# Kernel tuning notes

Measured on AMD Instinct MI355X. Metric: run time of the kernel, lower is better.

## Reference

```python
import jax, jax.numpy as jnp
import numpy as np

B, N, HID = 1, 2048, 1024
H, WK, WV = 16, 64, 64
DH = HID // H  # 64


def setup_inputs() -> dict:
    key = jax.random.key(0)
    ks = jax.random.split(key, 10)
    s = 0.02
    return {
        "hidden_states": jax.random.normal(ks[0], (B, N, HID), jnp.float32),
        "attention_mask": jnp.ones((B, N), jnp.float32),
        "Wq": jax.random.normal(ks[1], (HID, HID), jnp.float32) * s,
        "bq": jnp.zeros((HID,), jnp.float32),
        "Wk": jax.random.normal(ks[2], (HID, HID), jnp.float32) * s,
        "bk": jnp.zeros((HID,), jnp.float32),
        "Wv": jax.random.normal(ks[3], (HID, HID), jnp.float32) * s,
        "bv": jnp.zeros((HID,), jnp.float32),
        # Conv1D(2*WK+1, DH, bias=False): weight [nx=DH, nf=2*WK+1]
        "W_rel_k": jax.random.normal(ks[4], (DH, 2 * WK + 1), jnp.float32) * s,
        # relative_pos_val: [2*WV+1, DH]
        "W_rel_v": jax.random.normal(ks[5], (2 * WV + 1, DH), jnp.float32) * s,
    }


def _attention(hidden_states, attention_mask, Wq, bq, Wk, bk, Wv, bv, W_rel_k, W_rel_v):
    b, n, _ = hidden_states.shape

    def heads(x):  # [B,N,HID] -> [B,H,N,DH]
        return x.reshape(b, n, H, DH).transpose(0, 2, 1, 3)

    q = heads(hidden_states @ Wq + bq)
    k = heads(hidden_states @ Wk + bk)
    v = heads(hidden_states @ Wv + bv)

    scores = jnp.einsum("bhid,bhjd->bhij", q, k)  # [B,H,N,N]

    # --- relative-position key bias: bias[i, j] = q_i . w_{j-i+WK} for |j-i|<=WK ---
    a_k = jnp.einsum("bhid,dw->bhiw", q, W_rel_k)  # [B,H,N,2*WK+1]
    rows = jnp.arange(n)
    slot = rows[None, :] - rows[:, None] + WK       # [N,N] relative slot j-i+WK
    valid_k = (slot >= 0) & (slot <= 2 * WK)
    bias = a_k[:, :, rows[:, None], jnp.clip(slot, 0, 2 * WK)]  # [B,H,N,N]
    scores = scores + jnp.where(valid_k, bias, 0.0)

    scores = scores / np.float32(np.sqrt(DH))  # temperature == 1.0

    # extended attention mask: (1 - mask) * dtype_min added to scores
    ext = (1.0 - attention_mask)[:, None, None, :] * jnp.finfo(scores.dtype).min
    scores = scores + ext

    probs = jax.nn.softmax(scores, axis=-1)  # [B,H,N,N]

    ctx = jnp.einsum("bhij,bhjd->bhid", probs, v)  # [B,H,N,DH]

    # --- relative-position value: band[i, r] = probs[i, i-WV+r]; ctx += band @ W_rel_v ---
    offs = jnp.arange(2 * WV + 1)
    kpos = rows[:, None] - WV + offs[None, :]       # [N, 2*WV+1] absolute key position
    valid_v = (kpos >= 0) & (kpos < n)
    band = probs[:, :, rows[:, None], jnp.clip(kpos, 0, n - 1)]  # [B,H,N,2*WV+1]
    band = jnp.where(valid_v, band, 0.0)
    ctx = ctx + jnp.einsum("bhiw,wd->bhid", band, W_rel_v)

    # merge heads -> [B,N,HID]
    return ctx.transpose(0, 2, 1, 3).reshape(b, n, HID)


def reference(hidden_states, attention_mask, Wq, bq, Wk, bk, Wv, bv, W_rel_k, W_rel_v):
    return _attention(hidden_states, attention_mask, Wq, bq, Wk, bk, Wv, bv, W_rel_k, W_rel_v)
```

## Files before the change

kernel.cpp:

```cpp
#include <hip/hip_runtime.h>
#include <hip/hip_bf16.h>

#define NSEQ 2048
#define HIDDIM 1024
#define NH 16
#define DHEAD 64
#define NW 129
#define AKS 132

typedef float          f32x4 __attribute__((ext_vector_type(4)));
typedef _Float16       f16x4 __attribute__((ext_vector_type(4)));
typedef _Float16       f16x8 __attribute__((ext_vector_type(8)));
typedef unsigned short u16x8 __attribute__((ext_vector_type(8)));
typedef unsigned short u16;

__device__ __forceinline__ float b2f(u16 u){ return __uint_as_float(((unsigned)u) << 16); }
__device__ __forceinline__ float ld_any(const void* p, long idx, int flag){
  return flag ? b2f(((const u16*)p)[idx]) : ((const float*)p)[idx];
}

static const size_t OFF_Q    = 0;
static const size_t OFF_K    = (size_t)4  << 20;
static const size_t OFF_VT   = (size_t)8  << 20;
static const size_t OFF_WT   = (size_t)12 << 20;
static const size_t OFF_AK   = (size_t)18 << 20;
static const size_t OFF_M    = OFF_AK + (size_t)NH * NSEQ * AKS * 4;
static const size_t OFF_L    = OFF_M + (size_t)2 * NH * NSEQ * 4;
static const size_t OFF_CTXP = OFF_L + (size_t)2 * NH * NSEQ * 4;
static const size_t OFF_HSF  = OFF_CTXP + (size_t)2 * NSEQ * HIDDIM * 4;
static const size_t OFF_BIAS = OFF_HSF + (size_t)NSEQ * HIDDIM * 2;
static const size_t OFF_WRK  = OFF_BIAS + 3 * 1024 * 4;
static const size_t OFF_WRV  = OFF_WRK + (size_t)DHEAD * NW * 4;
static const size_t OFF_EXT  = OFF_WRV + (size_t)NW * DHEAD * 4;
static const size_t OFF_FLAG = OFF_EXT + (size_t)NSEQ * 4;

__global__ void detect_kernel(const unsigned* __restrict__ mask_raw, int* __restrict__ flagp){
  *flagp = (mask_raw[0] == 0x3F800000u) ? 0 : 1;
}

__global__ void cvt_hs_kernel(const void* __restrict__ hs, const int* __restrict__ flagp,
                              _Float16* __restrict__ hsf){
  const int flag = *flagp;
  const long base = (long)(blockIdx.x * 256 + threadIdx.x) * 8;
  f16x8 o;
  if (flag){
    const u16* b = (const u16*)hs;
#pragma unroll
    for (int e = 0; e < 8; e++) o[e] = (_Float16)b2f(b[base + e]);
  } else {
    const float* f = (const float*)hs;
#pragma unroll
    for (int e = 0; e < 8; e++) o[e] = (_Float16)f[base + e];
  }
  *(f16x8*)(hsf + base) = o;
}

__global__ void cvt_small_kernel(const void* __restrict__ bq, const void* __restrict__ bk,
                                 const void* __restrict__ bv, const void* __restrict__ wrk,
                                 const void* __restrict__ wrv, const void* __restrict__ mask,
                                 const int* __restrict__ flagp,
                                 float* __restrict__ biasf, float* __restrict__ wrkf,
                                 float* __restrict__ wrvf, float* __restrict__ extf){
  const int flag = *flagp;
  const int idx = blockIdx.x * 256 + threadIdx.x;
  if (idx < 1024)            biasf[idx] = ld_any(bq, idx, flag);
  else if (idx < 2048)       biasf[idx] = ld_any(bk, idx - 1024, flag);
  else if (idx < 3072)       biasf[idx] = ld_any(bv, idx - 2048, flag);
  else if (idx < 3072 + 8256)  wrkf[idx - 3072]  = ld_any(wrk, idx - 3072, flag);
  else if (idx < 3072 + 16512) wrvf[idx - 11328] = ld_any(wrv, idx - 11328, flag);
  else if (idx < 3072 + 16512 + 2048)
    extf[idx - 19584] = (1.f - ld_any(mask, idx - 19584, flag)) * -1.0e30f;
}

__global__ void wtrans_kernel(const void* __restrict__ Wq, const void* __restrict__ Wk,
                              const void* __restrict__ Wv, const int* __restrict__ flagp,
                              _Float16* __restrict__ Wt){
  __shared__ __attribute__((aligned(16))) _Float16 tile[64][65];
  const int flag = *flagp;
  const int z = blockIdx.z;
  const void* src = (z == 0) ? Wq : ((z == 1) ? Wk : Wv);
  _Float16* dst = Wt + (size_t)z * 1024 * 1024;
  const int o0 = blockIdx.x * 64, k0 = blockIdx.y * 64;
  const int t = threadIdx.x;
#pragma unroll
  for (int c = 0; c < 2; c++){
    int idx = t + 256 * c;
    int r = idx >> 3, c8 = (idx & 7) * 8;
    long off = (long)(k0 + r) * 1024 + o0 + c8;
#pragma unroll
    for (int e = 0; e < 8; e++) tile[r][c8 + e] = (_Float16)ld_any(src, off + e, flag);
  }
  __syncthreads();
#pragma unroll
  for (int c = 0; c < 2; c++){
    int idx = t + 256 * c;
    int orow = idx >> 3, k8 = (idx & 7) * 8;
    f16x8 v;
#pragma unroll
    for (int e = 0; e < 8; e++) v[e] = tile[k8 + e][orow];
    *(f16x8*)(dst + (size_t)(o0 + orow) * 1024 + k0 + k8) = v;
  }
}

__launch_bounds__(256, 2)
__global__ void qkv_kernel(const _Float16* __restrict__ hsf, const _Float16* __restrict__ Wt,
                           const float* __restrict__ biasf,
                           _Float16* __restrict__ Qf, _Float16* __restrict__ Kf,
                           _Float16* __restrict__ Vtf){
  __shared__ __attribute__((aligned(16))) _Float16 As[128 * 40];
  __shared__ __attribute__((aligned(16))) _Float16 Bs[128 * 40];
  const int z = blockIdx.z;
  const _Float16* Wz = Wt + (size_t)z * 1024 * 1024;
  const int o0 = blockIdx.x * 128, m0 = blockIdx.y * 128;
  const int t = threadIdx.x, lane = t & 63, wave = t >> 6;
  const int wm = wave >> 1, wn = wave & 1;
  const int q = lane >> 4, ln = lane & 15;
  f32x4 acc[4][4];
#pragma unroll
  for (int a = 0; a < 4; a++)
#pragma unroll
    for (int b = 0; b < 4; b++) acc[a][b] = (f32x4){0.f, 0.f, 0.f, 0.f};

  for (int k0 = 0; k0 < 1024; k0 += 32){
#pragma unroll
    for (int c = 0; c < 2; c++){
      int idx = t + 256 * c;
      int r = idx >> 2, col = (idx & 3) * 8;
      *(f16x8*)&As[r * 40 + col] = *(const f16x8*)(hsf + (size_t)(m0 + r) * 1024 + k0 + col);
      *(f16x8*)&Bs[r * 40 + col] = *(const f16x8*)(Wz + (size_t)(o0 + r) * 1024 + k0 + col);
    }
    __syncthreads();
    f16x8 af[4], bf[4];
#pragma unroll
    for (int mt = 0; mt < 4; mt++) af[mt] = *(const f16x8*)&As[(wm * 64 + mt * 16 + ln) * 40 + q * 8];
#pragma unroll
    for (int nt = 0; nt < 4; nt++) bf[nt] = *(const f16x8*)&Bs[(wn * 64 + nt * 16 + ln) * 40 + q * 8];
#pragma unroll
    for (int mt = 0; mt < 4; mt++)
#pragma unroll
      for (int nt = 0; nt < 4; nt++)
        acc[mt][nt] = __builtin_amdgcn_mfma_f32_16x16x32_f16(af[mt], bf[nt], acc[mt][nt], 0, 0, 0);
    __syncthreads();
  }
#pragma unroll
  for (int nt = 0; nt < 4; nt++){
    int o = o0 + wn * 64 + nt * 16 + ln;
    float bval = biasf[z * 1024 + o];
    int hh = o >> 6, dd = o & 63;
#pragma unroll
    for (int mt = 0; mt < 4; mt++){
      int nb = m0 + wm * 64 + mt * 16 + q * 4;
      if (z == 2){
        f16x4 pk;
#pragma unroll
        for (int r = 0; r < 4; r++) pk[r] = (_Float16)(acc[mt][nt][r] + bval);
        *(f16x4*)(Vtf + (size_t)(hh * 64 + dd) * 2048 + nb) = pk;
      } else {
        _Float16* dstp = (z == 0) ? Qf : Kf;
#pragma unroll
        for (int r = 0; r < 4; r++)
          dstp[(size_t)(hh * 2048 + nb + r) * 64 + dd] = (_Float16)(acc[mt][nt][r] + bval);
      }
    }
  }
}

__launch_bounds__(256, 2)
__global__ void ak_kernel(const _Float16* __restrict__ Qf, const float* __restrict__ wrkf,
                          float* __restrict__ ak){
  __shared__ __attribute__((aligned(16))) _Float16 WrkT[144 * 72];
  const int h = blockIdx.y;
  const int i0 = blockIdx.x * 128;
  const int t = threadIdx.x, lane = t & 63, wave = t >> 6;
  const int q = lane >> 4, ln = lane & 15;
  for (int c = 0; c < 36; c++){
    int idx = t + 256 * c;
    int w = idx >> 6, d = idx & 63;
    float v = (w < NW) ? wrkf[d * NW + w] : 0.f;
    WrkT[w * 72 + d] = (_Float16)v;
  }
  __syncthreads();
  f16x8 afr[2][2];
#pragma unroll
  for (int mt = 0; mt < 2; mt++){
    int row = i0 + wave * 32 + mt * 16 + ln;
#pragma unroll
    for (int ks = 0; ks < 2; ks++)
      afr[mt][ks] = *(const f16x8*)(Qf + (size_t)(h * 2048 + row) * 64 + ks * 32 + q * 8);
  }
  f32x4 acc[2][9];
#pragma unroll
  for (int a = 0; a < 2; a++)
#pragma unroll
    for (int b = 0; b < 9; b++) acc[a][b] = (f32x4){0.f, 0.f, 0.f, 0.f};
#pragma unroll
  for (int nt = 0; nt < 9; nt++){
    f16x8 bfr0 = *(const f16x8*)&WrkT[(nt * 16 + ln) * 72 + q * 8];
    f16x8 bfr1 = *(const f16x8*)&WrkT[(nt * 16 + ln) * 72 + 32 + q * 8];
#pragma unroll
    for (int mt = 0; mt < 2; mt++){
      acc[mt][nt] = __builtin_amdgcn_mfma_f32_16x16x32_f16(afr[mt][0], bfr0, acc[mt][nt], 0, 0, 0);
      acc[mt][nt] = __builtin_amdgcn_mfma_f32_16x16x32_f16(afr[mt][1], bfr1, acc[mt][nt], 0, 0, 0);
    }
  }
#pragma unroll
  for (int nt = 0; nt < 9; nt++){
    int w = nt * 16 + ln;
    if (w > 128) continue;
#pragma unroll
    for (int mt = 0; mt < 2; mt++){
      int ib = i0 + wave * 32 + mt * 16 + q * 4;
#pragma unroll
      for (int r = 0; r < 4; r++)
        ak[(size_t)(h * 2048 + ib + r) * AKS + w] = acc[mt][nt][r];
    }
  }
}

__launch_bounds__(256, 4)
__global__ void flash_kernel(const float* __restrict__ extf,
                             const _Float16* __restrict__ Qf, const _Float16* __restrict__ Kf,
                             const _Float16* __restrict__ Vtf, float* akm,
                             float* __restrict__ ctxpart, float* __restrict__ mws,
                             float* __restrict__ lws){
  __shared__ __attribute__((aligned(16))) _Float16 Ks[128 * 72];
  __shared__ __attribute__((aligned(16))) _Float16 Vts[64 * 136];
  __shared__ __attribute__((aligned(16))) float exts[128];
  const int h = blockIdx.x, qt = blockIdx.y, jh = blockIdx.z;
  const int t = threadIdx.x, lane = t & 63, wave = t >> 6;
  const int q = lane >> 4, ln = lane & 15;
  const int ibase = qt * 64 + wave * 16;
  const int i = ibase + ln;
  f16x8 qfrag[2];
  {
    const _Float16* qrow = Qf + (size_t)(h * 2048 + i) * 64;
    qfrag[0] = *(const f16x8*)(qrow + q * 8);
    qfrag[1] = *(const f16x8*)(qrow + 32 + q * 8);
  }
  f32x4 accc[4];
#pragma unroll
  for (int dt = 0; dt < 4; dt++) accc[dt] = (f32x4){0.f, 0.f, 0.f, 0.f};
  float m_i = -1.0e30f, l_i = 0.f;
  float* akrow = akm + (size_t)(h * 2048 + i) * AKS;

  for (int jt = 0; jt < 8; jt++){
    const int j0 = jh * 1024 + jt * 128;
#pragma unroll
    for (int c = 0; c < 4; c++){
      int idx = t + 256 * c;
      {
        int row = idx >> 3, col = idx & 7;
        *(f16x8*)&Ks[row * 72 + col * 8] =
            *(const f16x8*)(Kf + (size_t)(h * 2048 + j0 + row) * 64 + col * 8);
      }
      {
        int row = idx >> 4, col = idx & 15;
        *(f16x8*)&Vts[row * 136 + col * 8] =
            *(const f16x8*)(Vtf + (size_t)(h * 64 + row) * 2048 + j0 + col * 8);
      }
    }
    if (t < 128) exts[t] = extf[j0 + t];
    __syncthreads();
    f32x4 s[8];
#pragma unroll
    for (int mt = 0; mt < 8; mt++){
      f16x8 kf0 = *(const f16x8*)&Ks[(mt * 16 + ln) * 72 + q * 8];
      f16x8 kf1 = *(const f16x8*)&Ks[(mt * 16 + ln) * 72 + 32 + q * 8];
      f32x4 zz = (f32x4){0.f, 0.f, 0.f, 0.f};
      zz = __builtin_amdgcn_mfma_f32_16x16x32_f16(kf0, qfrag[0], zz, 0, 0, 0);
      zz = __builtin_amdgcn_mfma_f32_16x16x32_f16(kf1, qfrag[1], zz, 0, 0, 0);
      s[mt] = zz;
    }
    const bool band = (j0 <= ibase + 79) && (j0 + 127 >= ibase - 64);
#pragma unroll
    for (int mt = 0; mt < 8; mt++){
      f32x4 ev = *(const f32x4*)&exts[mt * 16 + q * 4];
#pragma unroll
      for (int r = 0; r < 4; r++){
        float x = s[mt][r];
        int w = j0 + mt * 16 + q * 4 + r - i + 64;
        if (band && (unsigned)w <= 128u){
          x = (x + akrow[w]) * 0.125f + ev[r];
          akrow[w] = x;
        } else {
          x = x * 0.125f + ev[r];
        }
        s[mt][r] = x;
      }
    }
    float tmax = -1.0e30f;
#pragma unroll
    for (int mt = 0; mt < 8; mt++)
#pragma unroll
      for (int r = 0; r < 4; r++) tmax = fmaxf(tmax, s[mt][r]);
    tmax = fmaxf(tmax, __shfl_xor(tmax, 16, 64));
    tmax = fmaxf(tmax, __shfl_xor(tmax, 32, 64));
    float mnew = fmaxf(m_i, tmax);
    float alpha = __expf(m_i - mnew);
    m_i = mnew;
    l_i *= alpha;
#pragma unroll
    for (int dt = 0; dt < 4; dt++)
#pragma unroll
      for (int r = 0; r < 4; r++) accc[dt][r] *= alpha;
    float tsum = 0.f;
    f16x4 pf[8];
#pragma unroll
    for (int mt = 0; mt < 8; mt++)
#pragma unroll
      for (int r = 0; r < 4; r++){
        float p = __expf(s[mt][r] - mnew);
        tsum += p;
        pf[mt][r] = (_Float16)p;
      }
    tsum += __shfl_xor(tsum, 16, 64);
    tsum += __shfl_xor(tsum, 32, 64);
    l_i += tsum;
#pragma unroll
    for (int dt = 0; dt < 4; dt++){
#pragma unroll
      for (int ks = 0; ks < 8; ks++){
        f16x4 vf = *(const f16x4*)&Vts[(dt * 16 + ln) * 136 + ks * 16 + q * 4];
        accc[dt] = __builtin_amdgcn_mfma_f32_16x16x16f16(vf, pf[ks], accc[dt], 0, 0, 0);
      }
    }
    __syncthreads();
  }
  float* cdst = ctxpart + (size_t)jh * NSEQ * HIDDIM;
#pragma unroll
  for (int dt = 0; dt < 4; dt++)
    *(f32x4*)(cdst + (size_t)i * 1024 + h * 64 + dt * 16 + q * 4) = accc[dt];
  if (q == 0){
    mws[jh * NH * NSEQ + h * 2048 + i] = m_i;
    lws[jh * NH * NSEQ + h * 2048 + i] = l_i;
  }
}

__launch_bounds__(256, 2)
__global__ void finish_kernel(const float* __restrict__ sband, const float* __restrict__ mws,
                              const float* __restrict__ lws, const float* __restrict__ wrvf,
                              const float* __restrict__ ctxpart, float* __restrict__ out){
  __shared__ __attribute__((aligned(16))) _Float16 WrvT[64 * 144];
  __shared__ __attribute__((aligned(16))) _Float16 pT[144 * 72];
  __shared__ __attribute__((aligned(16))) float sM[64], sIL[64], sC0[64], sC1[64];
  const int qt = blockIdx.x, h = blockIdx.y;
  const int i0 = qt * 64;
  const int t = threadIdx.x, lane = t & 63, wave = t >> 6;
  const int q = lane >> 4, ln = lane & 15;
  for (int c = 0; c < 36; c++){
    int idx = c * 256 + t;
    int w = idx >> 6, d = idx & 63;
    WrvT[d * 144 + w] = (w < NW) ? (_Float16)wrvf[w * 64 + d] : (_Float16)0.f;
  }
  if (t < 64){
    int i = i0 + t;
    float m0 = mws[h * 2048 + i],            m1 = mws[NH * NSEQ + h * 2048 + i];
    float l0 = lws[h * 2048 + i],            l1 = lws[NH * NSEQ + h * 2048 + i];
    float M = fmaxf(m0, m1);
    float a0 = __expf(m0 - M), a1 = __expf(m1 - M);
    float L = a0 * l0 + a1 * l1;
    float iL = 1.f / L;
    sM[t] = M; sIL[t] = iL; sC0[t] = a0 * iL; sC1[t] = a1 * iL;
  }
  __syncthreads();
  for (int ii = 0; ii < 16; ii++){
    int il = wave * 16 + ii;
    float Mv = sM[il], ILv = sIL[il];
    const float* srow = sband + (size_t)(h * 2048 + i0 + il) * AKS;
#pragma unroll
    for (int c = 0; c < 3; c++){
      int w = lane + 64 * c;
      if (w < 144){
        float p = (w < NW) ? __expf(srow[w] - Mv) * ILv : 0.f;
        pT[w * 72 + il] = (_Float16)p;
      }
    }
  }
  __syncthreads();
  f32x4 acc[4];
#pragma unroll
  for (int mt = 0; mt < 4; mt++) acc[mt] = (f32x4){0.f, 0.f, 0.f, 0.f};
#pragma unroll
  for (int ks = 0; ks < 9; ks++){
    f16x4 bfr;
#pragma unroll
    for (int j = 0; j < 4; j++) bfr[j] = pT[(ks * 16 + q * 4 + j) * 72 + wave * 16 + ln];
#pragma unroll
    for (int mt = 0; mt < 4; mt++){
      f16x4 afr = *(const f16x4*)&WrvT[(mt * 16 + ln) * 144 + ks * 16 + q * 4];
      acc[mt] = __builtin_amdgcn_mfma_f32_16x16x16f16(afr, bfr, acc[mt], 0, 0, 0);
    }
  }
  const int i = i0 + wave * 16 + ln;
  const float c0 = sC0[wave * 16 + ln], c1 = sC1[wave * 16 + ln];
  const float* p0 = ctxpart;
  const float* p1 = ctxpart + (size_t)NSEQ * HIDDIM;
#pragma unroll
  for (int mt = 0; mt < 4; mt++){
    size_t off = (size_t)i * 1024 + h * 64 + mt * 16 + q * 4;
    f32x4 A0 = *(const f32x4*)(p0 + off);
    f32x4 A1 = *(const f32x4*)(p1 + off);
    f32x4 o4;
#pragma unroll
    for (int r = 0; r < 4; r++) o4[r] = c0 * A0[r] + c1 * A1[r] + acc[mt][r];
    *(f32x4*)(out + off) = o4;
  }
}

extern "C" void kernel_launch(void* const* d_in, const int* in_sizes, int n_in,
                              void* d_out, int out_size, void* d_ws, size_t ws_size,
                              hipStream_t stream){
  const void* hs   = d_in[0];
  const void* mask = d_in[1];
  const void* Wq   = d_in[2];
  const void* bq   = d_in[3];
  const void* Wk   = d_in[4];
  const void* bk   = d_in[5];
  const void* Wv   = d_in[6];
  const void* bv   = d_in[7];
  const void* Wrk  = d_in[8];
  const void* Wrv  = d_in[9];
  float* out = (float*)d_out;

  char* ws = (char*)d_ws;
  _Float16* Qf    = (_Float16*)(ws + OFF_Q);
  _Float16* Kf    = (_Float16*)(ws + OFF_K);
  _Float16* Vtf   = (_Float16*)(ws + OFF_VT);
  _Float16* Wt    = (_Float16*)(ws + OFF_WT);
  float*    akp   = (float*)   (ws + OFF_AK);
  float*    mp    = (float*)   (ws + OFF_M);
  float*    lp    = (float*)   (ws + OFF_L);
  float*    ctxp  = (float*)   (ws + OFF_CTXP);
  _Float16* hsf   = (_Float16*)(ws + OFF_HSF);
  float*    biasf = (float*)   (ws + OFF_BIAS);
  float*    wrkf  = (float*)   (ws + OFF_WRK);
  float*    wrvf  = (float*)   (ws + OFF_WRV);
  float*    extf  = (float*)   (ws + OFF_EXT);
  int*      flagp = (int*)     (ws + OFF_FLAG);

  detect_kernel   <<<dim3(1),          1,   0, stream>>>((const unsigned*)mask, flagp);
  cvt_hs_kernel   <<<dim3(1024),       256, 0, stream>>>(hs, flagp, hsf);
  cvt_small_kernel<<<dim3(85),         256, 0, stream>>>(bq, bk, bv, Wrk, Wrv, mask, flagp,
                                                         biasf, wrkf, wrvf, extf);
  wtrans_kernel   <<<dim3(16, 16, 3),  256, 0, stream>>>(Wq, Wk, Wv, flagp, Wt);
  qkv_kernel      <<<dim3(8, 16, 3),   256, 0, stream>>>(hsf, Wt, biasf, Qf, Kf, Vtf);
  ak_kernel       <<<dim3(16, 16),     256, 0, stream>>>(Qf, wrkf, akp);
  flash_kernel    <<<dim3(16, 32, 2),  256, 0, stream>>>(extf, Qf, Kf, Vtf, akp, ctxp, mp, lp);
  finish_kernel   <<<dim3(32, 16),     256, 0, stream>>>(akp, mp, lp, wrvf, ctxp, out);
}
```

Baseline: 208.4 us.

## Merge prep kernels, register-prefetch tiles in QKV and flash, compute row sums via MFMA

Four preprocessing launches (detect, hs convert, small convert, weight transpose) become one prep kernel that finds the dtype flag inline, cutting launch overhead. The QKV GEMM and flash kernel now prefetch the next K/V/ext tile into registers while the current tile is being computed, overlapping global loads with MFMA work. The flash kernel also appends a ones-row to the V^T shared tile so an extra MFMA tile yields the softmax denominator, which removes the per-tile shuffle reductions. The cost is more register pressure and an extra fifth MFMA column per step, and the row sum is now built from fp16-rounded probabilities.

New measurement: 211.1 us. Within noise of the previous version (+1.3%).

```diff
diff --git a/kernel.cpp b/kernel.cpp
--- a/kernel.cpp
+++ b/kernel.cpp
@@ -7,6 +7,7 @@
 #define DHEAD 64
 #define NW 129
 #define AKS 132
+#define VTS 132
 
 typedef float          f32x4 __attribute__((ext_vector_type(4)));
 typedef _Float16       f16x4 __attribute__((ext_vector_type(4)));
@@ -32,73 +33,65 @@
 static const size_t OFF_WRK  = OFF_BIAS + 3 * 1024 * 4;
 static const size_t OFF_WRV  = OFF_WRK + (size_t)DHEAD * NW * 4;
 static const size_t OFF_EXT  = OFF_WRV + (size_t)NW * DHEAD * 4;
-static const size_t OFF_FLAG = OFF_EXT + (size_t)NSEQ * 4;
-
-__global__ void detect_kernel(const unsigned* __restrict__ mask_raw, int* __restrict__ flagp){
-  *flagp = (mask_raw[0] == 0x3F800000u) ? 0 : 1;
-}
-
-__global__ void cvt_hs_kernel(const void* __restrict__ hs, const int* __restrict__ flagp,
-                              _Float16* __restrict__ hsf){
-  const int flag = *flagp;
-  const long base = (long)(blockIdx.x * 256 + threadIdx.x) * 8;
-  f16x8 o;
-  if (flag){
-    const u16* b = (const u16*)hs;
-#pragma unroll
-    for (int e = 0; e < 8; e++) o[e] = (_Float16)b2f(b[base + e]);
+
+__global__ void prep_kernel(const void* __restrict__ hs,
+                            const void* __restrict__ Wq, const void* __restrict__ Wk,
+                            const void* __restrict__ Wv,
+                            const void* __restrict__ bq, const void* __restrict__ bk,
+                            const void* __restrict__ bv, const void* __restrict__ wrk,
+                            const void* __restrict__ wrv, const void* __restrict__ mask,
+                            _Float16* __restrict__ hsf, _Float16* __restrict__ Wt,
+                            float* __restrict__ biasf, float* __restrict__ wrkf,
+                            float* __restrict__ wrvf, float* __restrict__ extf){
+  __shared__ __attribute__((aligned(16))) _Float16 tile[64][65];
+  const int flag = (((const unsigned*)mask)[0] == 0x3F800000u) ? 0 : 1;
+  const int b = blockIdx.x, t = threadIdx.x;
+  if (b < 1024){
+    const long base = (long)(b * 256 + t) * 8;
+    f16x8 o;
+    if (flag){
+      const u16* src = (const u16*)hs;
+#pragma unroll
+      for (int e = 0; e < 8; e++) o[e] = (_Float16)b2f(src[base + e]);
+    } else {
+      const float* src = (const float*)hs;
+#pragma unroll
+      for (int e = 0; e < 8; e++) o[e] = (_Float16)src[base + e];
+    }
+    *(f16x8*)(hsf + base) = o;
+  } else if (b < 1792){
+    const int b2 = b - 1024;
+    const int z = b2 >> 8, r = b2 & 255;
+    const int o0 = (r & 15) * 64, k0 = (r >> 4) * 64;
+    const void* src = (z == 0) ? Wq : ((z == 1) ? Wk : Wv);
+    _Float16* dst = Wt + (size_t)z * 1024 * 1024;
+#pragma unroll
+    for (int c = 0; c < 2; c++){
+      int idx = t + 256 * c;
+      int rr = idx >> 3, c8 = (idx & 7) * 8;
+      long off = (long)(k0 + rr) * 1024 + o0 + c8;
+#pragma unroll
+      for (int e = 0; e < 8; e++) tile[rr][c8 + e] = (_Float16)ld_any(src, off + e, flag);
+    }
+    __syncthreads();
+#pragma unroll
+    for (int c = 0; c < 2; c++){
+      int idx = t + 256 * c;
+      int orow = idx >> 3, k8 = (idx & 7) * 8;
+      f16x8 v;
+#pragma unroll
+      for (int e = 0; e < 8; e++) v[e] = tile[k8 + e][orow];
+      *(f16x8*)(dst + (size_t)(o0 + orow) * 1024 + k0 + k8) = v;
+    }
   } else {
-    const float* f = (const float*)hs;
-#pragma unroll
-    for (int e = 0; e < 8; e++) o[e] = (_Float16)f[base + e];
-  }
-  *(f16x8*)(hsf + base) = o;
-}
-
-__global__ void cvt_small_kernel(const void* __restrict__ bq, const void* __restrict__ bk,
-                                 const void* __restrict__ bv, const void* __restrict__ wrk,
-                                 const void* __restrict__ wrv, const void* __restrict__ mask,
-                                 const int* __restrict__ flagp,
-                                 float* __restrict__ biasf, float* __restrict__ wrkf,
-                                 float* __restrict__ wrvf, float* __restrict__ extf){
-  const int flag = *flagp;
-  const int idx = blockIdx.x * 256 + threadIdx.x;
-  if (idx < 1024)            biasf[idx] = ld_any(bq, idx, flag);
-  else if (idx < 2048)       biasf[idx] = ld_any(bk, idx - 1024, flag);
-  else if (idx < 3072)       biasf[idx] = ld_any(bv, idx - 2048, flag);
-  else if (idx < 3072 + 8256)  wrkf[idx - 3072]  = ld_any(wrk, idx - 3072, flag);
-  else if (idx < 3072 + 16512) wrvf[idx - 11328] = ld_any(wrv, idx - 11328, flag);
-  else if (idx < 3072 + 16512 + 2048)
-    extf[idx - 19584] = (1.f - ld_any(mask, idx - 19584, flag)) * -1.0e30f;
-}
-
-__global__ void wtrans_kernel(const void* __restrict__ Wq, const void* __restrict__ Wk,
-                              const void* __restrict__ Wv, const int* __restrict__ flagp,
-                              _Float16* __restrict__ Wt){
-  __shared__ __attribute__((aligned(16))) _Float16 tile[64][65];
-  const int flag = *flagp;
-  const int z = blockIdx.z;
-  const void* src = (z == 0) ? Wq : ((z == 1) ? Wk : Wv);
-  _Float16* dst = Wt + (size_t)z * 1024 * 1024;
-  const int o0 = blockIdx.x * 64, k0 = blockIdx.y * 64;
-  const int t = threadIdx.x;
-#pragma unroll
-  for (int c = 0; c < 2; c++){
-    int idx = t + 256 * c;
-    int r = idx >> 3, c8 = (idx & 7) * 8;
-    long off = (long)(k0 + r) * 1024 + o0 + c8;
-#pragma unroll
-    for (int e = 0; e < 8; e++) tile[r][c8 + e] = (_Float16)ld_any(src, off + e, flag);
-  }
-  __syncthreads();
-#pragma unroll
-  for (int c = 0; c < 2; c++){
-    int idx = t + 256 * c;
-    int orow = idx >> 3, k8 = (idx & 7) * 8;
-    f16x8 v;
-#pragma unroll
-    for (int e = 0; e < 8; e++) v[e] = tile[k8 + e][orow];
-    *(f16x8*)(dst + (size_t)(o0 + orow) * 1024 + k0 + k8) = v;
+    const int idx = (b - 1792) * 256 + t;
+    if (idx < 1024)            biasf[idx] = ld_any(bq, idx, flag);
+    else if (idx < 2048)       biasf[idx] = ld_any(bk, idx - 1024, flag);
+    else if (idx < 3072)       biasf[idx] = ld_any(bv, idx - 2048, flag);
+    else if (idx < 3072 + 8256)  wrkf[idx - 3072]  = ld_any(wrk, idx - 3072, flag);
+    else if (idx < 3072 + 16512) wrvf[idx - 11328] = ld_any(wrv, idx - 11328, flag);
+    else if (idx < 3072 + 16512 + 2048)
+      extf[idx - 19584] = (1.f - ld_any(mask, idx - 19584, flag)) * -1.0e30f;
   }
 }
 
@@ -115,21 +108,33 @@
   const int t = threadIdx.x, lane = t & 63, wave = t >> 6;
   const int wm = wave >> 1, wn = wave & 1;
   const int q = lane >> 4, ln = lane & 15;
+  const int srow = t >> 2, scol = (t & 3) * 8;
   f32x4 acc[4][4];
 #pragma unroll
   for (int a = 0; a < 4; a++)
 #pragma unroll
     for (int b = 0; b < 4; b++) acc[a][b] = (f32x4){0.f, 0.f, 0.f, 0.f};
 
+  f16x8 ar[2], br[2];
+#pragma unroll
+  for (int c = 0; c < 2; c++){
+    ar[c] = *(const f16x8*)(hsf + (size_t)(m0 + srow + 64 * c) * 1024 + scol);
+    br[c] = *(const f16x8*)(Wz + (size_t)(o0 + srow + 64 * c) * 1024 + scol);
+  }
   for (int k0 = 0; k0 < 1024; k0 += 32){
 #pragma unroll
     for (int c = 0; c < 2; c++){
-      int idx = t + 256 * c;
-      int r = idx >> 2, col = (idx & 3) * 8;
-      *(f16x8*)&As[r * 40 + col] = *(const f16x8*)(hsf + (size_t)(m0 + r) * 1024 + k0 + col);
-      *(f16x8*)&Bs[r * 40 + col] = *(const f16x8*)(Wz + (size_t)(o0 + r) * 1024 + k0 + col);
+      *(f16x8*)&As[(srow + 64 * c) * 40 + scol] = ar[c];
+      *(f16x8*)&Bs[(srow + 64 * c) * 40 + scol] = br[c];
     }
     __syncthreads();
+    if (k0 + 32 < 1024){
+#pragma unroll
+      for (int c = 0; c < 2; c++){
+        ar[c] = *(const f16x8*)(hsf + (size_t)(m0 + srow + 64 * c) * 1024 + k0 + 32 + scol);
+        br[c] = *(const f16x8*)(Wz + (size_t)(o0 + srow + 64 * c) * 1024 + k0 + 32 + scol);
+      }
+    }
     f16x8 af[4], bf[4];
 #pragma unroll
     for (int mt = 0; mt < 4; mt++) af[mt] = *(const f16x8*)&As[(wm * 64 + mt * 16 + ln) * 40 + q * 8];
@@ -224,7 +229,7 @@
                              float* __restrict__ ctxpart, float* __restrict__ mws,
                              float* __restrict__ lws){
   __shared__ __attribute__((aligned(16))) _Float16 Ks[128 * 72];
-  __shared__ __attribute__((aligned(16))) _Float16 Vts[64 * 136];
+  __shared__ __attribute__((aligned(16))) _Float16 Vts[80 * VTS];
   __shared__ __attribute__((aligned(16))) float exts[128];
   const int h = blockIdx.x, qt = blockIdx.y, jh = blockIdx.z;
   const int t = threadIdx.x, lane = t & 63, wave = t >> 6;
@@ -237,30 +242,48 @@
     qfrag[0] = *(const f16x8*)(qrow + q * 8);
     qfrag[1] = *(const f16x8*)(qrow + 32 + q * 8);
   }
-  f32x4 accc[4];
-#pragma unroll
-  for (int dt = 0; dt < 4; dt++) accc[dt] = (f32x4){0.f, 0.f, 0.f, 0.f};
-  float m_i = -1.0e30f, l_i = 0.f;
+  for (int k = t; k < 16 * VTS; k += 256){
+    int rr = k / VTS, cc = k - rr * VTS;
+    Vts[(64 + rr) * VTS + cc] = (rr == 0 && cc < 128) ? (_Float16)1.f : (_Float16)0.f;
+  }
+  f32x4 accc[5];
+#pragma unroll
+  for (int dt = 0; dt < 5; dt++) accc[dt] = (f32x4){0.f, 0.f, 0.f, 0.f};
+  float m_i = -1.0e30f;
   float* akrow = akm + (size_t)(h * 2048 + i) * AKS;
+  const int jbase = jh * 1024;
+  const int krow = t >> 3, kcol = (t & 7) * 8;
+  const int vrow = t >> 4, vcol = (t & 15) * 8;
+
+  f16x8 kr[4], vr[4]; float er = 0.f;
+#pragma unroll
+  for (int c = 0; c < 4; c++){
+    kr[c] = *(const f16x8*)(Kf + (size_t)(h * 2048 + jbase + krow + 32 * c) * 64 + kcol);
+    vr[c] = *(const f16x8*)(Vtf + (size_t)(h * 64 + vrow + 16 * c) * 2048 + jbase + vcol);
+  }
+  if (t < 128) er = extf[jbase + t];
 
   for (int jt = 0; jt < 8; jt++){
-    const int j0 = jh * 1024 + jt * 128;
+    const int j0 = jbase + jt * 128;
 #pragma unroll
     for (int c = 0; c < 4; c++){
-      int idx = t + 256 * c;
-      {
-        int row = idx >> 3, col = idx & 7;
-        *(f16x8*)&Ks[row * 72 + col * 8] =
-            *(const f16x8*)(Kf + (size_t)(h * 2048 + j0 + row) * 64 + col * 8);
-      }
-      {
-        int row = idx >> 4, col = idx & 15;
-        *(f16x8*)&Vts[row * 136 + col * 8] =
-            *(const f16x8*)(Vtf + (size_t)(h * 64 + row) * 2048 + j0 + col * 8);
-      }
-    }
-    if (t < 128) exts[t] = extf[j0 + t];
+      *(f16x8*)&Ks[(krow + 32 * c) * 72 + kcol] = kr[c];
+      f16x4 lo = {vr[c][0], vr[c][1], vr[c][2], vr[c][3]};
+      f16x4 hi = {vr[c][4], vr[c][5], vr[c][6], vr[c][7]};
+      *(f16x4*)&Vts[(vrow + 16 * c) * VTS + vcol] = lo;
+      *(f16x4*)&Vts[(vrow + 16 * c) * VTS + vcol + 4] = hi;
+    }
+    if (t < 128) exts[t] = er;
     __syncthreads();
+    if (jt < 7){
+      const int j1 = j0 + 128;
+#pragma unroll
+      for (int c = 0; c < 4; c++){
+        kr[c] = *(const f16x8*)(Kf + (size_t)(h * 2048 + j1 + krow + 32 * c) * 64 + kcol);
+        vr[c] = *(const f16x8*)(Vtf + (size_t)(h * 64 + vrow + 16 * c) * 2048 + j1 + vcol);
+      }
+      if (t < 128) er = extf[j1 + t];
+    }
     f32x4 s[8];
 #pragma unroll
     for (int mt = 0; mt < 8; mt++){
@@ -298,29 +321,21 @@
     float mnew = fmaxf(m_i, tmax);
     float alpha = __expf(m_i - mnew);
     m_i = mnew;
-    l_i *= alpha;
-#pragma unroll
-    for (int dt = 0; dt < 4; dt++)
+#pragma unroll
+    for (int dt = 0; dt < 5; dt++)
 #pragma unroll
       for (int r = 0; r < 4; r++) accc[dt][r] *= alpha;
-    float tsum = 0.f;
     f16x4 pf[8];
 #pragma unroll
     for (int mt = 0; mt < 8; mt++)
 #pragma unroll
-      for (int r = 0; r < 4; r++){
-        float p = __expf(s[mt][r] - mnew);
-        tsum += p;
-        pf[mt][r] = (_Float16)p;
-      }
-    tsum += __shfl_xor(tsum, 16, 64);
-    tsum += __shfl_xor(tsum, 32, 64);
-    l_i += tsum;
-#pragma unroll
-    for (int dt = 0; dt < 4; dt++){
+      for (int r = 0; r < 4; r++)
+        pf[mt][r] = (_Float16)__expf(s[mt][r] - mnew);
+#pragma unroll
+    for (int dt = 0; dt < 5; dt++){
 #pragma unroll
       for (int ks = 0; ks < 8; ks++){
-        f16x4 vf = *(const f16x4*)&Vts[(dt * 16 + ln) * 136 + ks * 16 + q * 4];
+        f16x4 vf = *(const f16x4*)&Vts[(dt * 16 + ln) * VTS + ks * 16 + q * 4];
         accc[dt] = __builtin_amdgcn_mfma_f32_16x16x16f16(vf, pf[ks], accc[dt], 0, 0, 0);
       }
     }
@@ -332,7 +347,7 @@
     *(f32x4*)(cdst + (size_t)i * 1024 + h * 64 + dt * 16 + q * 4) = accc[dt];
   if (q == 0){
     mws[jh * NH * NSEQ + h * 2048 + i] = m_i;
-    lws[jh * NH * NSEQ + h * 2048 + i] = l_i;
+    lws[jh * NH * NSEQ + h * 2048 + i] = accc[4][0];
   }
 }
 
@@ -436,15 +451,11 @@
   float*    wrkf  = (float*)   (ws + OFF_WRK);
   float*    wrvf  = (float*)   (ws + OFF_WRV);
   float*    extf  = (float*)   (ws + OFF_EXT);
-  int*      flagp = (int*)     (ws + OFF_FLAG);
-
-  detect_kernel   <<<dim3(1),          1,   0, stream>>>((const unsigned*)mask, flagp);
-  cvt_hs_kernel   <<<dim3(1024),       256, 0, stream>>>(hs, flagp, hsf);
-  cvt_small_kernel<<<dim3(85),         256, 0, stream>>>(bq, bk, bv, Wrk, Wrv, mask, flagp,
-                                                         biasf, wrkf, wrvf, extf);
-  wtrans_kernel   <<<dim3(16, 16, 3),  256, 0, stream>>>(Wq, Wk, Wv, flagp, Wt);
-  qkv_kernel      <<<dim3(8, 16, 3),   256, 0, stream>>>(hsf, Wt, biasf, Qf, Kf, Vtf);
-  ak_kernel       <<<dim3(16, 16),     256, 0, stream>>>(Qf, wrkf, akp);
-  flash_kernel    <<<dim3(16, 32, 2),  256, 0, stream>>>(extf, Qf, Kf, Vtf, akp, ctxp, mp, lp);
-  finish_kernel   <<<dim3(32, 16),     256, 0, stream>>>(akp, mp, lp, wrvf, ctxp, out);
-}
+
+  prep_kernel  <<<dim3(1877),      256, 0, stream>>>(hs, Wq, Wk, Wv, bq, bk, bv, Wrk, Wrv, mask,
+                                                     hsf, Wt, biasf, wrkf, wrvf, extf);
+  qkv_kernel   <<<dim3(8, 16, 3),  256, 0, stream>>>(hsf, Wt, biasf, Qf, Kf, Vtf);
+  ak_kernel    <<<dim3(16, 16),    256, 0, stream>>>(Qf, wrkf, akp);
+  flash_kernel <<<dim3(16, 32, 2), 256, 0, stream>>>(extf, Qf, Kf, Vtf, akp, ctxp, mp, lp);
+  finish_kernel<<<dim3(32, 16),    256, 0, stream>>>(akp, mp, lp, wrvf, ctxp, out);
+}
```
